# Kernel tuning notes

Measured on AMD Instinct MI355X. Metric: run time of the kernel, lower is better.

## Reference

```python
import jax, jax.numpy as jnp
import numpy as np

B, T, H, L, AS = 64, 256, 1024, 3, 128  # batch, seq-1, hidden, layers, alphabet


def setup_inputs() -> dict:
    key = jax.random.key(0)
    ks = jax.random.split(key, 8)
    # one-hot character sequence (B, T, AS), float32
    idx = jax.random.randint(ks[0], (B, T), 0, AS)
    sequence = jax.nn.one_hot(idx, AS, dtype=jnp.float32)
    u = lambda k, shape, fan: jax.random.uniform(
        k, shape, minval=-1.0 / np.sqrt(fan), maxval=1.0 / np.sqrt(fan), dtype=jnp.float32)
    W_i2h = u(ks[1], (H, AS), AS)
    b_i2h = u(ks[2], (H,), AS)
    # per-layer LSTM params, PyTorch gate order [i, f, g, o]; layer inputs all have width H
    W_ih = u(ks[3], (L, 4 * H, H), H)
    W_hh = u(ks[4], (L, 4 * H, H), H)
    b_ih = u(ks[5], (L, 4 * H), H)
    b_hh = u(ks[6], (L, 4 * H), H)
    W_h2O = u(ks[7], (AS, H), H)
    b_h2O = jnp.zeros((AS,), dtype=jnp.float32)
    h0 = jnp.zeros((L, B, H), dtype=jnp.float32)
    c0 = jnp.zeros((L, B, H), dtype=jnp.float32)
    return dict(sequence=sequence, W_i2h=W_i2h, b_i2h=b_i2h, W_ih=W_ih, W_hh=W_hh,
                b_ih=b_ih, b_hh=b_hh, W_h2O=W_h2O, b_h2O=b_h2O, h0=h0, c0=c0)


def _lstm_layer(x, h0, c0, W_ih, W_hh, b_ih, b_hh):
    # x: (B, T, H). Precompute input contribution to the gates for all steps.
    xg = jnp.einsum('bth,gh->btg', x, W_ih) + b_ih  # (B, T, 4H)

    def step(carry, xg_t):
        h, c = carry
        gates = xg_t + h @ W_hh.T + b_hh  # (B, 4H)
        i, f, g, o = jnp.split(gates, 4, axis=-1)
        c = jax.nn.sigmoid(f) * c + jax.nn.sigmoid(i) * jnp.tanh(g)
        h = jax.nn.sigmoid(o) * jnp.tanh(c)
        return (h, c), h

    (hT, cT), hs = jax.lax.scan(step, (h0, c0), jnp.swapaxes(xg, 0, 1))
    return jnp.swapaxes(hs, 0, 1), hT, cT  # (B,T,H), (B,H), (B,H)


def reference(sequence, W_i2h, b_i2h, W_ih, W_hh, b_ih, b_hh, W_h2O, b_h2O, h0, c0):
    # i2h projection
    x = jnp.einsum('bta,ha->bth', sequence, W_i2h) + b_i2h  # (B, T, H)
    # multi-layer LSTM over x (eval mode: the dropout=True arg is inactive in eval)
    inp = x
    h_fin, c_fin = [], []
    for l in range(L):
        inp, hT, cT = _lstm_layer(inp, h0[l], c0[l], W_ih[l], W_hh[l], b_ih[l], b_hh[l])
        h_fin.append(hT)
        c_fin.append(cT)
    # NOTE: faithful to the original code's bug -- h2O is applied to the i2h
    # output `x`, not to the LSTM output. The LSTM only produces the new hidden.
    out = x.reshape(-1, H) @ W_h2O.T + b_h2O  # (B*T, AS)
    return out, jnp.stack(h_fin), jnp.stack(c_fin)
```

## Files before the change

kernel.cpp:

```cpp
#include <hip/hip_runtime.h>
#include <stdint.h>
#include <stddef.h>

#define B_  64
#define T_  256
#define H_  1024
#define AS_ 128
#define L_  3

typedef __attribute__((ext_vector_type(8))) short bf16x8;
typedef __attribute__((ext_vector_type(4))) float f32x4;
typedef __attribute__((ext_vector_type(4))) unsigned u32x4;

__device__ __forceinline__ unsigned short f2bf(float f) {
  union { float f; unsigned u; } x; x.f = f;
  unsigned r = x.u + 0x7fffu + ((x.u >> 16) & 1u);
  return (unsigned short)(r >> 16);
}
__device__ __forceinline__ float bf2f(unsigned short s) {
  union { unsigned u; float f; } x; x.u = ((unsigned)s) << 16; return x.f;
}
__device__ __forceinline__ float sigmf(float x) { return 1.0f / (1.0f + __expf(-x)); }
__device__ __forceinline__ float tanh_f(float x) {
  x = fminf(fmaxf(x, -15.0f), 15.0f);
  float e = __expf(2.0f * x);
  return (e - 1.0f) / (e + 1.0f);
}

__device__ __forceinline__ void st_u16_cc(unsigned short* p, unsigned short v) {
  __hip_atomic_store(p, v, __ATOMIC_RELAXED, __HIP_MEMORY_SCOPE_AGENT);
}
__device__ __forceinline__ void st_u32_cc(unsigned* p, unsigned v) {
  __hip_atomic_store(p, v, __ATOMIC_RELAXED, __HIP_MEMORY_SCOPE_AGENT);
}
__device__ __forceinline__ unsigned ld_u32_cc(const unsigned* p) {
  return __hip_atomic_load(p, __ATOMIC_RELAXED, __HIP_MEMORY_SCOPE_AGENT);
}
__device__ __forceinline__ u32x4 ld_b128_cc_nw(const void* p) {
  u32x4 r;
  asm volatile("global_load_dwordx4 %0, %1, off sc0 sc1" : "=v"(r) : "v"(p));
  return r;
}
__device__ __forceinline__ unsigned long long ld_b64_cc_nw(const void* p) {
  unsigned long long r;
  asm volatile("global_load_dwordx2 %0, %1, off sc0 sc1" : "=v"(r) : "v"(p));
  return r;
}
__device__ __forceinline__ void st_b128_cc_nw(void* p, u32x4 v) {
  asm volatile("global_store_dwordx4 %0, %1, off sc0 sc1" :: "v"(p), "v"(v) : "memory");
}
__device__ __forceinline__ void wait_vm4_tie6(u32x4& a, u32x4& b, u32x4& c, u32x4& d,
                                              unsigned long long& x, unsigned long long& y) {
  asm volatile("s_waitcnt vmcnt(4)"
               : "+v"(a), "+v"(b), "+v"(c), "+v"(d), "+v"(x), "+v"(y) :: "memory");
  __builtin_amdgcn_sched_barrier(0);
}
__device__ __forceinline__ void wait_vm0_tie4(u32x4& a, u32x4& b, u32x4& c, u32x4& d) {
  asm volatile("s_waitcnt vmcnt(0)"
               : "+v"(a), "+v"(b), "+v"(c), "+v"(d) :: "memory");
  __builtin_amdgcn_sched_barrier(0);
}
__device__ __forceinline__ void lds_barrier() {
  __builtin_amdgcn_sched_barrier(0);
  asm volatile("s_waitcnt lgkmcnt(0)" ::: "memory");
  __builtin_amdgcn_sched_barrier(0);
  __builtin_amdgcn_s_barrier();
  __builtin_amdgcn_sched_barrier(0);
}


__global__ void k_prep(unsigned* __restrict__ zp, int nzero,
                       const float* __restrict__ Wi2h, const float* __restrict__ bi2h,
                       unsigned short* __restrict__ Wt,
                       const float* __restrict__ Wih, unsigned short* __restrict__ Wihb, int nwih,
                       const float* __restrict__ Wh2o, unsigned short* __restrict__ Wh2ob,
                       const float* __restrict__ bih, const float* __restrict__ bhh,
                       float* __restrict__ bsum) {
  int i = blockIdx.x * 256 + threadIdx.x;
  if (i < nzero) { st_u32_cc(zp + i, 0u); return; }
  i -= nzero;
  if (i < AS_ * H_) { int a = i >> 10, h = i & 1023; Wt[i] = f2bf(Wi2h[h * AS_ + a] + bi2h[h]); return; }
  i -= AS_ * H_;
  if (i < nwih) { Wihb[i] = f2bf(Wih[i]); return; }
  i -= nwih;
  if (i < AS_ * H_) { Wh2ob[i] = f2bf(Wh2o[i]); return; }
  i -= AS_ * H_;
  if (i < L_ * 4 * H_) bsum[i] = bih[i] + bhh[i];
}

__global__ __launch_bounds__(128) void k_gather(const float* __restrict__ seq,
                                                const unsigned short* __restrict__ Wt,
                                                unsigned short* __restrict__ xbf) {
  __shared__ int sidx;
  const int bt = blockIdx.x, tid = threadIdx.x;
  if (seq[(size_t)bt * AS_ + tid] > 0.5f) sidx = tid;
  __syncthreads();
  const int b = bt >> 8, t = bt & 255;
  const uint4* s = (const uint4*)(Wt + (size_t)sidx * H_);
  uint4* d = (uint4*)(xbf + ((size_t)t * B_ + b) * H_);
  d[tid] = s[tid];
}


__device__ __forceinline__ void gld16(const void* g, void* l) {
  __builtin_amdgcn_global_load_lds((const __attribute__((address_space(1))) unsigned int*)g,
                                   (__attribute__((address_space(3))) unsigned int*)l,
                                   16, 0, 0);
}

template <int OUT>
__device__ __forceinline__ void gemm_tile(const unsigned short* __restrict__ A,
                                          const unsigned short* __restrict__ Bm,
                                          const float* __restrict__ bias,
                                          void* __restrict__ Cout,
                                          int m0, int n0, int K, int N, int tid,
                                          unsigned short* As, unsigned short* Bs) {
  const int lane = tid & 63, wv = tid >> 6;
  const int wr = wv >> 1, wc = wv & 1;
  const int kg = lane >> 4, li = lane & 15;
  f32x4 acc[4][4] = {};

  for (int k0 = 0; k0 < K; k0 += 32) {
    for (int i = 0; i < 2; ++i) {
      int c0 = i * 256 + wv * 64;
      int cid = c0 + lane;
      int row = cid >> 2, lc = cid & 3;
      int sc = lc ^ ((row >> 1) & 3);
      gld16(A + (size_t)(m0 + row) * K + k0 + sc * 8, (char*)As + (size_t)c0 * 16);
      gld16(Bm + (size_t)(n0 + row) * K + k0 + sc * 8, (char*)Bs + (size_t)c0 * 16);
    }
    __syncthreads();
    bf16x8 af[4], bfm[4];
#pragma unroll
    for (int mi = 0; mi < 4; ++mi) {
      int row = wr * 64 + mi * 16 + li;
      int pc = kg ^ ((row >> 1) & 3);
      af[mi] = *(const bf16x8*)((const char*)As + row * 64 + pc * 16);
    }
#pragma unroll
    for (int ni = 0; ni < 4; ++ni) {
      int row = wc * 64 + ni * 16 + li;
      int pc = kg ^ ((row >> 1) & 3);
      bfm[ni] = *(const bf16x8*)((const char*)Bs + row * 64 + pc * 16);
    }
#pragma unroll
    for (int mi = 0; mi < 4; ++mi)
#pragma unroll
      for (int ni = 0; ni < 4; ++ni)
        acc[mi][ni] = __builtin_amdgcn_mfma_f32_16x16x32_bf16(af[mi], bfm[ni], acc[mi][ni], 0, 0, 0);
    __syncthreads();
  }

#pragma unroll
  for (int mi = 0; mi < 4; ++mi)
#pragma unroll
    for (int ni = 0; ni < 4; ++ni)
#pragma unroll
      for (int r = 0; r < 4; ++r) {
        int row = m0 + wr * 64 + mi * 16 + kg * 4 + r;
        int col = n0 + wc * 64 + ni * 16 + li;
        float v = acc[mi][ni][r] + bias[col];
        int tt = row >> 6, b = row & 63;
        if (OUT == 4) {
          ((float*)Cout)[(size_t)(b * 256 + tt) * N + col] = v;
        } else {
          int g = col >> 10, u = col & 1023;
          int idx = ((tt * 4 + (b >> 4)) << 16) | ((u >> 5) << 11) |
                    ((b & 15) << 7) | ((u & 31) << 2) | g;
          if (OUT == 3) st_u16_cc(&((unsigned short*)Cout)[idx], f2bf(v));
          else          ((unsigned short*)Cout)[idx] = f2bf(v);
        }
      }
}


__global__ __launch_bounds__(256, 1) void k_fused(
    const unsigned short* __restrict__ xgs,
    const float* __restrict__ Whh,
    unsigned short* __restrict__ h_pp,
    unsigned short* __restrict__ out_seq,
    float* __restrict__ hT, float* __restrict__ cT,
    const float* __restrict__ h0, const float* __restrict__ c0,
    unsigned* __restrict__ slots,
    const unsigned short* __restrict__ WihbN,
    const float* __restrict__ bsumN,
    unsigned short* __restrict__ xgs_out,
    const unsigned short* __restrict__ xg0A,
    const unsigned short* __restrict__ Wihb0,
    const float* __restrict__ bsum0,
    unsigned* __restrict__ xgprog,
    const unsigned short* __restrict__ WoutB,
    const float* __restrict__ bout,
    float* __restrict__ outC) {
  __shared__ __align__(16) unsigned short Wlds[64 * 1024];
  __shared__ __align__(16) unsigned short Hs[16 * 1024];
  const int tid = threadIdx.x, lane = tid & 63, w = tid >> 6;
  const int wg = blockIdx.x;

  if (wg >= 128) {
    const int Wp = wg - 128;
    unsigned short* As = Wlds;
    unsigned short* Bs = Wlds + 4096;
    if (xg0A) {
      for (int k = 0; k < 32; ++k) {
        const int gidx = k * 128 + Wp;
        gemm_tile<3>(xg0A, Wihb0, bsum0, (void*)xgs_out,
                     (gidx >> 5) * 128, (gidx & 31) * 128, H_, 4 * H_, tid, As, Bs);
        asm volatile("s_waitcnt vmcnt(0)" ::: "memory");
        __syncthreads();
        if (tid == 0) {
          st_u32_cc(&xgprog[Wp], (unsigned)(k + 1));
          asm volatile("s_waitcnt vmcnt(0)" ::: "memory");
        }
      }
      gemm_tile<4>(xg0A, WoutB, bout, (void*)outC, Wp * 128, 0, H_, AS_, tid, As, Bs);
    }
    if (WihbN) {
      const int pline = (Wp & 31) * 32;
      for (int k = 0; k < 32; ++k) {
        const int gidx = Wp + k * 128;
        const int mt = gidx >> 5, nt = gidx & 31;
        const unsigned tgt = (unsigned)(2 * mt + 3);
        if (w == 0) {
          const unsigned* base = slots + (lane >> 4) * 1024 + pline + (lane & 15);
          unsigned v0, v1;
          do {
            __builtin_amdgcn_s_sleep(4);
            v0 = ld_u32_cc(base);
            v1 = ld_u32_cc(base + 16);
          } while (__any((int)((v0 < tgt) | (v1 < tgt))));
        }
        __syncthreads();
        gemm_tile<2>(out_seq, WihbN, bsumN, (void*)xgs_out,
                     mt * 128, nt * 128, H_, 4 * H_, tid, As, Bs);
      }
    }
    return;
  }

  const int gb = wg >> 5, ug = wg & 31;
  const int li = lane & 15, kq = lane >> 4;
  const int b  = gb * 16 + li;
  const int u0 = ug * 32 + w * 8 + kq;
  const int u1 = u0 + 4;

  st_u16_cc(&h_pp[((size_t)B_ + b) * H_ + u0], f2bf(h0[(size_t)b * H_ + u0]));
  st_u16_cc(&h_pp[((size_t)B_ + b) * H_ + u1], f2bf(h0[(size_t)b * H_ + u1]));

  bf16x8 afr[32];
  {
    const int r0 = w * 32 + li;
    const float* wr = Whh + ((size_t)(r0 & 3) * H_ + ug * 32 + (r0 >> 2)) * H_ + kq * 8;
#pragma unroll
    for (int ks = 0; ks < 32; ++ks) {
      const float4 f0 = *(const float4*)(wr + ks * 32);
      const float4 f1 = *(const float4*)(wr + ks * 32 + 4);
      union { ushort4 a[2]; bf16x8 v; } uu_;
      uu_.a[0] = ushort4{f2bf(f0.x), f2bf(f0.y), f2bf(f0.z), f2bf(f0.w)};
      uu_.a[1] = ushort4{f2bf(f1.x), f2bf(f1.y), f2bf(f1.z), f2bf(f1.w)};
      afr[ks] = uu_.v;
    }
  }
  for (int it = 0; it < 16; ++it) {
    const int r = w * 32 + 16 + it;
    const float* wr = Whh + ((size_t)(r & 3) * H_ + ug * 32 + (r >> 2)) * H_;
#pragma unroll
    for (int j = 0; j < 4; ++j) {
      const float4 f = *(const float4*)(wr + lane * 16 + j * 4);
      ushort4 p = ushort4{f2bf(f.x), f2bf(f.y), f2bf(f.z), f2bf(f.w)};
      const int k = lane * 16 + j * 4;
      *(ushort4*)((char*)Wlds + (size_t)(w * 16 + it) * 2048 + ((2 * k) ^ ((it & 7) << 4))) = p;
    }
  }
  float cs0 = c0[(size_t)b * H_ + u0], cs1 = c0[(size_t)b * H_ + u1];
  __syncthreads();
  if (w == 3 && lane < 32) {
    st_u32_cc(&slots[gb * 1024 + lane * 32 + ug], 1u);
    asm volatile("s_waitcnt vmcnt(0)" ::: "memory");
  }

  const char* hbase = (const char*)Hs + (size_t)li * 2048;
  const char* wlb   = (const char*)Wlds + (size_t)(w * 16 + li) * 2048;
  const int fxor = (li & 7) << 4;
  const int sb = tid >> 4, seg = tid & 15;
  const int sswz = (sb & 7) << 4;
  char* drow = (char*)Hs + (size_t)sb * 2048;
  unsigned short* exch = Hs;
  const unsigned* myline = slots + gb * 1024 + ug * 32;

  for (int t = 0; t < T_; ++t) {
    if (w == 0) {
      const unsigned tgt = (unsigned)(t + 1);
      const int mt = t >> 1;
      const unsigned gtgt = (unsigned)((mt >> 2) + 1);
      const unsigned* gp = xgprog ? (xgprog + (mt & 3) * 32 + (lane & 31)) : nullptr;
      unsigned v, g;
      do {
        __builtin_amdgcn_s_sleep(1);
        v = ld_u32_cc(&myline[lane & 31]);
        g = gp ? ld_u32_cc(gp) : 0x7FFFFFFFu;
      } while (__any((int)((v < tgt) | (g < gtgt))));
    }
    __syncthreads();

    const size_t xb2 = ((((size_t)t * 4 + gb) << 16) | (ug << 11) | (li << 7) |
                        ((w * 8 + kq) << 2)) * 2;
    unsigned long long xar = ld_b64_cc_nw((const char*)xgs + xb2);
    unsigned long long xbr = ld_b64_cc_nw((const char*)xgs + xb2 + 32);
    const char* srcrow = (const char*)(h_pp + (size_t)((t & 1) ^ 1) * (B_ * H_) +
                                       (size_t)(gb * 16 + sb) * H_);
    u32x4 A0 = ld_b128_cc_nw(srcrow +   0 * 256 + seg * 16);
    u32x4 A1 = ld_b128_cc_nw(srcrow +   1 * 256 + seg * 16);
    u32x4 A2 = ld_b128_cc_nw(srcrow +   2 * 256 + seg * 16);
    u32x4 A3 = ld_b128_cc_nw(srcrow +   3 * 256 + seg * 16);
    u32x4 B0 = ld_b128_cc_nw(srcrow + 1024 + 0 * 256 + seg * 16);
    u32x4 B1 = ld_b128_cc_nw(srcrow + 1024 + 1 * 256 + seg * 16);
    u32x4 B2 = ld_b128_cc_nw(srcrow + 1024 + 2 * 256 + seg * 16);
    u32x4 B3 = ld_b128_cc_nw(srcrow + 1024 + 3 * 256 + seg * 16);
    wait_vm4_tie6(A0, A1, A2, A3, xar, xbr);
    *(u32x4*)(drow + ((0 * 256 + seg * 16) ^ sswz)) = A0;
    *(u32x4*)(drow + ((1 * 256 + seg * 16) ^ sswz)) = A1;
    *(u32x4*)(drow + ((2 * 256 + seg * 16) ^ sswz)) = A2;
    *(u32x4*)(drow + ((3 * 256 + seg * 16) ^ sswz)) = A3;
    lds_barrier();

    f32x4 a0 = {0.f, 0.f, 0.f, 0.f}, a1 = {0.f, 0.f, 0.f, 0.f};
#pragma unroll
    for (int ks = 0; ks < 16; ++ks) {
      const bf16x8 bb = *(const bf16x8*)(hbase + ((ks * 64 + kq * 16) ^ fxor));
      a0 = __builtin_amdgcn_mfma_f32_16x16x32_bf16(afr[ks], bb, a0, 0, 0, 0);
      const bf16x8 aw = *(const bf16x8*)(wlb + ((ks * 64 + kq * 16) ^ fxor));
      a1 = __builtin_amdgcn_mfma_f32_16x16x32_bf16(aw, bb, a1, 0, 0, 0);
    }

    wait_vm0_tie4(B0, B1, B2, B3);
    *(u32x4*)(drow + ((1024 + 0 * 256 + seg * 16) ^ sswz)) = B0;
    *(u32x4*)(drow + ((1024 + 1 * 256 + seg * 16) ^ sswz)) = B1;
    *(u32x4*)(drow + ((1024 + 2 * 256 + seg * 16) ^ sswz)) = B2;
    *(u32x4*)(drow + ((1024 + 3 * 256 + seg * 16) ^ sswz)) = B3;
    lds_barrier();

#pragma unroll
    for (int ks = 16; ks < 32; ++ks) {
      const bf16x8 bb = *(const bf16x8*)(hbase + ((ks * 64 + kq * 16) ^ fxor));
      a0 = __builtin_amdgcn_mfma_f32_16x16x32_bf16(afr[ks], bb, a0, 0, 0, 0);
      const bf16x8 aw = *(const bf16x8*)(wlb + ((ks * 64 + kq * 16) ^ fxor));
      a1 = __builtin_amdgcn_mfma_f32_16x16x32_bf16(aw, bb, a1, 0, 0, 0);
    }

    const ushort4 xa = *(const ushort4*)&xar;
    const ushort4 xb = *(const ushort4*)&xbr;
    float h0v, h1v;
    {
      float gi = a0[0] + bf2f(xa.x), gf = a0[1] + bf2f(xa.y);
      float gg = a0[2] + bf2f(xa.z), go = a0[3] + bf2f(xa.w);
      float ci = sigmf(gf) * cs0 + sigmf(gi) * tanh_f(gg);
      cs0 = ci; h0v = sigmf(go) * tanh_f(ci);
    }
    {
      float gi = a1[0] + bf2f(xb.x), gf = a1[1] + bf2f(xb.y);
      float gg = a1[2] + bf2f(xb.z), go = a1[3] + bf2f(xb.w);
      float ci = sigmf(gf) * cs1 + sigmf(gi) * tanh_f(gg);
      cs1 = ci; h1v = sigmf(go) * tanh_f(ci);
    }
    const unsigned short hb0 = f2bf(h0v), hb1 = f2bf(h1v);

    __syncthreads();
    exch[li * 32 + w * 8 + kq]     = hb0;
    exch[li * 32 + w * 8 + kq + 4] = hb1;
    __syncthreads();

    if (t < T_ - 1) {
      const int bl = tid >> 4, j = tid & 15;
      const unsigned pack = (unsigned)exch[bl * 32 + 2 * j] |
                            ((unsigned)exch[bl * 32 + 2 * j + 1] << 16);
      st_u32_cc((unsigned*)&h_pp[((size_t)(t & 1) * B_ + gb * 16 + bl) * H_ + ug * 32 + 2 * j],
                pack);
    } else {
      hT[(size_t)b * H_ + u0] = h0v; hT[(size_t)b * H_ + u1] = h1v;
      cT[(size_t)b * H_ + u0] = cs0; cT[(size_t)b * H_ + u1] = cs1;
    }
    if (out_seq && tid < 64) {
      const int bo = tid >> 2, q = tid & 3;
      st_b128_cc_nw(&out_seq[((size_t)t * B_ + gb * 16 + bo) * H_ + ug * 32 + 8 * q],
                    *(const u32x4*)&exch[bo * 32 + 8 * q]);
    }
    asm volatile("s_waitcnt vmcnt(0)" ::: "memory");
    __syncthreads();
    if (w == 3 && lane < 32) {
      st_u32_cc(&slots[gb * 1024 + lane * 32 + ug], (unsigned)(t + 2));
      asm volatile("s_waitcnt vmcnt(0)" ::: "memory");
    }
  }
}


extern "C" void kernel_launch(void* const* d_in, const int* in_sizes, int n_in,
                              void* d_out, int out_size, void* d_ws, size_t ws_size,
                              hipStream_t stream) {
  const float* seq  = (const float*)d_in[0];
  const float* Wi2h = (const float*)d_in[1];
  const float* bi2h = (const float*)d_in[2];
  const float* Wih  = (const float*)d_in[3];
  const float* Whh  = (const float*)d_in[4];
  const float* bih  = (const float*)d_in[5];
  const float* bhh  = (const float*)d_in[6];
  const float* Wh2o = (const float*)d_in[7];
  const float* bh2o = (const float*)d_in[8];
  const float* h0   = (const float*)d_in[9];
  const float* c0   = (const float*)d_in[10];
  float* outF = (float*)d_out;

  size_t off = 0;
  auto nb = [&](size_t bytes) { size_t r = off; off += (bytes + 255) & ~(size_t)255; return r; };
  unsigned short* xbf   = (unsigned short*)((char*)d_ws + nb((size_t)B_ * T_ * H_ * 2));
  unsigned short* seqA  = (unsigned short*)((char*)d_ws + nb((size_t)B_ * T_ * H_ * 2));
  unsigned short* xgs   = (unsigned short*)((char*)d_ws + nb((size_t)B_ * T_ * 4 * H_ * 2));
  unsigned short* Wihb  = (unsigned short*)((char*)d_ws + nb((size_t)L_ * 4 * H_ * H_ * 2));
  unsigned short* Wh2ob = (unsigned short*)((char*)d_ws + nb((size_t)AS_ * H_ * 2));
  unsigned short* Wt    = (unsigned short*)((char*)d_ws + nb((size_t)AS_ * H_ * 2));
  float*          bsum  = (float*)((char*)d_ws + nb((size_t)L_ * 4 * H_ * 4));
  unsigned short* h_pp  = (unsigned short*)((char*)d_ws + nb((size_t)2 * B_ * H_ * 2));
  unsigned*       slt   = (unsigned*)((char*)d_ws + nb((size_t)(L_ * 4096 + 128) * 4));
  unsigned*       xgp   = slt + L_ * 4096;
  (void)ws_size; (void)in_sizes; (void)n_in; (void)out_size;

  const int WLAYER = 4 * H_ * H_;
  const int nzero = L_ * 4096 + 128;
  const int nprep = nzero + 2 * AS_ * H_ + L_ * WLAYER + L_ * 4 * H_;

  k_prep<<<(nprep + 255) / 256, 256, 0, stream>>>(
      slt, nzero, Wi2h, bi2h, Wt, Wih, Wihb, L_ * WLAYER, Wh2o, Wh2ob, bih, bhh, bsum);
  k_gather<<<B_ * T_, 128, 0, stream>>>(seq, Wt, xbf);

  float* hT_base = outF + (size_t)B_ * T_ * AS_;
  float* cT_base = hT_base + (size_t)L_ * B_ * H_;

  k_fused<<<256, 256, 0, stream>>>(
      xgs, Whh, h_pp, seqA,
      hT_base, cT_base, h0, c0, slt,
      Wihb + (size_t)1 * WLAYER, bsum + (size_t)1 * 4 * H_, xgs,
      xbf, Wihb, bsum, xgp, Wh2ob, bh2o, outF);

  k_fused<<<256, 256, 0, stream>>>(
      xgs, Whh + (size_t)1 * WLAYER, h_pp, xbf,
      hT_base + (size_t)B_ * H_, cT_base + (size_t)B_ * H_,
      h0 + (size_t)B_ * H_, c0 + (size_t)B_ * H_, slt + (size_t)4096,
      Wihb + (size_t)2 * WLAYER, bsum + (size_t)2 * 4 * H_, xgs,
      nullptr, nullptr, nullptr, nullptr, nullptr, nullptr, nullptr);

  k_fused<<<128, 256, 0, stream>>>(
      xgs, Whh + (size_t)2 * WLAYER, h_pp, nullptr,
      hT_base + (size_t)2 * B_ * H_, cT_base + (size_t)2 * B_ * H_,
      h0 + (size_t)2 * B_ * H_, c0 + (size_t)2 * B_ * H_, slt + (size_t)2 * 4096,
      nullptr, nullptr, nullptr, nullptr, nullptr, nullptr, nullptr, nullptr, nullptr, nullptr);
}
```

Baseline: 3.538 ms.

## Move layer-0 input-gate GEMM out of the fused recurrent kernel into a standalone launch

The layer-0 input projection (x @ W_ih^T) was computed inside the first recurrent kernel by 128 extra workgroups, with per-tile progress counters the recurrent workgroups polled before each step. It now runs as a separate full-grid GEMM kernel before the recurrence. The recurrent loop drops the xgprog poll and reads the gate inputs with plain loads issued before the spin-wait. This removes the polling and cross-workgroup coupling and lets the GEMM use the whole GPU. The cost is that the GEMM no longer overlaps with the layer-0 recurrence, adding its full time to the serial path.

Result: faster. 3.453 ms (-2.4%).

```diff
diff --git a/kernel.cpp b/kernel.cpp
--- a/kernel.cpp
+++ b/kernel.cpp
@@ -41,18 +41,12 @@
   asm volatile("global_load_dwordx4 %0, %1, off sc0 sc1" : "=v"(r) : "v"(p));
   return r;
 }
-__device__ __forceinline__ unsigned long long ld_b64_cc_nw(const void* p) {
-  unsigned long long r;
-  asm volatile("global_load_dwordx2 %0, %1, off sc0 sc1" : "=v"(r) : "v"(p));
-  return r;
-}
 __device__ __forceinline__ void st_b128_cc_nw(void* p, u32x4 v) {
   asm volatile("global_store_dwordx4 %0, %1, off sc0 sc1" :: "v"(p), "v"(v) : "memory");
 }
-__device__ __forceinline__ void wait_vm4_tie6(u32x4& a, u32x4& b, u32x4& c, u32x4& d,
-                                              unsigned long long& x, unsigned long long& y) {
+__device__ __forceinline__ void wait_vm4_tie4(u32x4& a, u32x4& b, u32x4& c, u32x4& d) {
   asm volatile("s_waitcnt vmcnt(4)"
-               : "+v"(a), "+v"(b), "+v"(c), "+v"(d), "+v"(x), "+v"(y) :: "memory");
+               : "+v"(a), "+v"(b), "+v"(c), "+v"(d) :: "memory");
   __builtin_amdgcn_sched_barrier(0);
 }
 __device__ __forceinline__ void wait_vm0_tie4(u32x4& a, u32x4& b, u32x4& c, u32x4& d) {
@@ -167,10 +161,21 @@
           int g = col >> 10, u = col & 1023;
           int idx = ((tt * 4 + (b >> 4)) << 16) | ((u >> 5) << 11) |
                     ((b & 15) << 7) | ((u & 31) << 2) | g;
-          if (OUT == 3) st_u16_cc(&((unsigned short*)Cout)[idx], f2bf(v));
-          else          ((unsigned short*)Cout)[idx] = f2bf(v);
+          ((unsigned short*)Cout)[idx] = f2bf(v);
         }
       }
+}
+
+template <int OUT>
+__global__ __launch_bounds__(256) void k_gemm(const unsigned short* __restrict__ A,
+                                              const unsigned short* __restrict__ Bm,
+                                              const float* __restrict__ bias,
+                                              void* __restrict__ Cout,
+                                              int M, int N, int K) {
+  __shared__ __align__(16) unsigned short As[128 * 32];
+  __shared__ __align__(16) unsigned short Bs[128 * 32];
+  gemm_tile<OUT>(A, Bm, bias, Cout, blockIdx.x * 128, blockIdx.y * 128,
+                 K, N, threadIdx.x, As, Bs);
 }
 
 
@@ -185,10 +190,7 @@
     const unsigned short* __restrict__ WihbN,
     const float* __restrict__ bsumN,
     unsigned short* __restrict__ xgs_out,
-    const unsigned short* __restrict__ xg0A,
-    const unsigned short* __restrict__ Wihb0,
-    const float* __restrict__ bsum0,
-    unsigned* __restrict__ xgprog,
+    const unsigned short* __restrict__ outA,
     const unsigned short* __restrict__ WoutB,
     const float* __restrict__ bout,
     float* __restrict__ outC) {
@@ -201,20 +203,8 @@
     const int Wp = wg - 128;
     unsigned short* As = Wlds;
     unsigned short* Bs = Wlds + 4096;
-    if (xg0A) {
-      for (int k = 0; k < 32; ++k) {
-        const int gidx = k * 128 + Wp;
-        gemm_tile<3>(xg0A, Wihb0, bsum0, (void*)xgs_out,
-                     (gidx >> 5) * 128, (gidx & 31) * 128, H_, 4 * H_, tid, As, Bs);
-        asm volatile("s_waitcnt vmcnt(0)" ::: "memory");
-        __syncthreads();
-        if (tid == 0) {
-          st_u32_cc(&xgprog[Wp], (unsigned)(k + 1));
-          asm volatile("s_waitcnt vmcnt(0)" ::: "memory");
-        }
-      }
-      gemm_tile<4>(xg0A, WoutB, bout, (void*)outC, Wp * 128, 0, H_, AS_, tid, As, Bs);
-    }
+    if (outA)
+      gemm_tile<4>(outA, WoutB, bout, (void*)outC, Wp * 128, 0, H_, AS_, tid, As, Bs);
     if (WihbN) {
       const int pline = (Wp & 31) * 32;
       for (int k = 0; k < 32; ++k) {
@@ -289,24 +279,21 @@
   const unsigned* myline = slots + gb * 1024 + ug * 32;
 
   for (int t = 0; t < T_; ++t) {
+    const size_t xb2 = ((((size_t)t * 4 + gb) << 16) | (ug << 11) | (li << 7) |
+                        ((w * 8 + kq) << 2)) * 2;
+    const ushort4 xa = *(const ushort4*)((const char*)xgs + xb2);
+    const ushort4 xb = *(const ushort4*)((const char*)xgs + xb2 + 32);
+
     if (w == 0) {
       const unsigned tgt = (unsigned)(t + 1);
-      const int mt = t >> 1;
-      const unsigned gtgt = (unsigned)((mt >> 2) + 1);
-      const unsigned* gp = xgprog ? (xgprog + (mt & 3) * 32 + (lane & 31)) : nullptr;
-      unsigned v, g;
+      unsigned v;
       do {
         __builtin_amdgcn_s_sleep(1);
         v = ld_u32_cc(&myline[lane & 31]);
-        g = gp ? ld_u32_cc(gp) : 0x7FFFFFFFu;
-      } while (__any((int)((v < tgt) | (g < gtgt))));
-    }
-    __syncthreads();
-
-    const size_t xb2 = ((((size_t)t * 4 + gb) << 16) | (ug << 11) | (li << 7) |
-                        ((w * 8 + kq) << 2)) * 2;
-    unsigned long long xar = ld_b64_cc_nw((const char*)xgs + xb2);
-    unsigned long long xbr = ld_b64_cc_nw((const char*)xgs + xb2 + 32);
+      } while (__any((int)(v < tgt)));
+    }
+    __syncthreads();
+
     const char* srcrow = (const char*)(h_pp + (size_t)((t & 1) ^ 1) * (B_ * H_) +
                                        (size_t)(gb * 16 + sb) * H_);
     u32x4 A0 = ld_b128_cc_nw(srcrow +   0 * 256 + seg * 16);
@@ -317,7 +304,7 @@
     u32x4 B1 = ld_b128_cc_nw(srcrow + 1024 + 1 * 256 + seg * 16);
     u32x4 B2 = ld_b128_cc_nw(srcrow + 1024 + 2 * 256 + seg * 16);
     u32x4 B3 = ld_b128_cc_nw(srcrow + 1024 + 3 * 256 + seg * 16);
-    wait_vm4_tie6(A0, A1, A2, A3, xar, xbr);
+    wait_vm4_tie4(A0, A1, A2, A3);
     *(u32x4*)(drow + ((0 * 256 + seg * 16) ^ sswz)) = A0;
     *(u32x4*)(drow + ((1 * 256 + seg * 16) ^ sswz)) = A1;
     *(u32x4*)(drow + ((2 * 256 + seg * 16) ^ sswz)) = A2;
@@ -348,8 +335,6 @@
       a1 = __builtin_amdgcn_mfma_f32_16x16x32_bf16(aw, bb, a1, 0, 0, 0);
     }
 
-    const ushort4 xa = *(const ushort4*)&xar;
-    const ushort4 xb = *(const ushort4*)&xbr;
     float h0v, h1v;
     {
       float gi = a0[0] + bf2f(xa.x), gf = a0[1] + bf2f(xa.y);
@@ -421,17 +406,19 @@
   unsigned short* Wt    = (unsigned short*)((char*)d_ws + nb((size_t)AS_ * H_ * 2));
   float*          bsum  = (float*)((char*)d_ws + nb((size_t)L_ * 4 * H_ * 4));
   unsigned short* h_pp  = (unsigned short*)((char*)d_ws + nb((size_t)2 * B_ * H_ * 2));
-  unsigned*       slt   = (unsigned*)((char*)d_ws + nb((size_t)(L_ * 4096 + 128) * 4));
-  unsigned*       xgp   = slt + L_ * 4096;
+  unsigned*       slt   = (unsigned*)((char*)d_ws + nb((size_t)L_ * 4096 * 4));
   (void)ws_size; (void)in_sizes; (void)n_in; (void)out_size;
 
   const int WLAYER = 4 * H_ * H_;
-  const int nzero = L_ * 4096 + 128;
+  const int nzero = L_ * 4096;
   const int nprep = nzero + 2 * AS_ * H_ + L_ * WLAYER + L_ * 4 * H_;
 
   k_prep<<<(nprep + 255) / 256, 256, 0, stream>>>(
       slt, nzero, Wi2h, bi2h, Wt, Wih, Wihb, L_ * WLAYER, Wh2o, Wh2ob, bih, bhh, bsum);
   k_gather<<<B_ * T_, 128, 0, stream>>>(seq, Wt, xbf);
+
+  k_gemm<2><<<dim3(B_ * T_ / 128, 4 * H_ / 128), 256, 0, stream>>>(
+      xbf, Wihb, bsum, (void*)xgs, B_ * T_, 4 * H_, H_);
 
   float* hT_base = outF + (size_t)B_ * T_ * AS_;
   float* cT_base = hT_base + (size_t)L_ * B_ * H_;
@@ -440,18 +427,18 @@
       xgs, Whh, h_pp, seqA,
       hT_base, cT_base, h0, c0, slt,
       Wihb + (size_t)1 * WLAYER, bsum + (size_t)1 * 4 * H_, xgs,
-      xbf, Wihb, bsum, xgp, Wh2ob, bh2o, outF);
+      xbf, Wh2ob, bh2o, outF);
 
   k_fused<<<256, 256, 0, stream>>>(
       xgs, Whh + (size_t)1 * WLAYER, h_pp, xbf,
       hT_base + (size_t)B_ * H_, cT_base + (size_t)B_ * H_,
       h0 + (size_t)B_ * H_, c0 + (size_t)B_ * H_, slt + (size_t)4096,
       Wihb + (size_t)2 * WLAYER, bsum + (size_t)2 * 4 * H_, xgs,
-      nullptr, nullptr, nullptr, nullptr, nullptr, nullptr, nullptr);
+      nullptr, nullptr, nullptr, nullptr);
 
   k_fused<<<128, 256, 0, stream>>>(
       xgs, Whh + (size_t)2 * WLAYER, h_pp, nullptr,
       hT_base + (size_t)2 * B_ * H_, cT_base + (size_t)2 * B_ * H_,
       h0 + (size_t)2 * B_ * H_, c0 + (size_t)2 * B_ * H_, slt + (size_t)2 * 4096,
-      nullptr, nullptr, nullptr, nullptr, nullptr, nullptr, nullptr, nullptr, nullptr, nullptr);
-}
+      nullptr, nullptr, nullptr, nullptr, nullptr, nullptr, nullptr);
+}
```
